# Kernel tuning notes

Hardware: AMD Instinct MI355X
Metric: run time of the kernel (lower is better)

## Reference

```python
import jax, jax.numpy as jnp
import numpy as np

B, N, DIM = 2, 2048, 512
H, DH = 8, 64
INNER = H * DH
SCALE = DH ** -0.5


def setup_inputs() -> dict:
    key = jax.random.key(0)
    ks = jax.random.split(key, 8)
    s = 0.02
    return {
        "nodes": jax.random.normal(ks[0], (B, N, DIM), dtype=jnp.float32),
        "edge_mask": jax.random.bernoulli(ks[1], 0.9, (B, N, N)),
        "wq": jax.random.normal(ks[2], (DIM, INNER), dtype=jnp.float32) * s,
        "bq": jnp.zeros((INNER,), dtype=jnp.float32),
        "wkv": jax.random.normal(ks[3], (DIM, 2 * INNER), dtype=jnp.float32) * s,
        "bkv": jnp.zeros((2 * INNER,), dtype=jnp.float32),
        "wo": jax.random.normal(ks[4], (INNER, DIM), dtype=jnp.float32) * s,
        "bo": jnp.zeros((DIM,), dtype=jnp.float32),
    }


def reference(nodes, edge_mask, wq, bq, wkv, bkv, wo, bo):
    b, n, _ = nodes.shape
    q = nodes @ wq + bq                      # [b, n, h*dh]
    kv = nodes @ wkv + bkv                   # [b, n, 2*h*dh]
    k, v = jnp.split(kv, 2, axis=-1)
    # split heads -> [b, h, n, dh]
    split = lambda t: t.reshape(b, n, H, DH).transpose(0, 2, 1, 3)
    q, k, v = split(q), split(k), split(v)
    sim = jnp.einsum('bhid,bhjd->bhij', q, k) * SCALE
    max_neg = -jnp.finfo(sim.dtype).max
    sim = jnp.where(edge_mask[:, None, :, :], sim, max_neg)
    attn = jax.nn.softmax(sim, axis=-1)
    out = jnp.einsum('bhij,bhjd->bhid', attn, v)      # [b, h, n, dh]
    out = out.transpose(0, 2, 1, 3).reshape(b, n, INNER)
    return out @ wo + bo
```

## Files before the change

### kernel.cpp

```cpp
#include <hip/hip_runtime.h>
#include <cstdint>
#include <cstddef>

#define DEVI __device__ __forceinline__

typedef __bf16 bf16x8 __attribute__((ext_vector_type(8)));
typedef float floatx4 __attribute__((ext_vector_type(4)));
typedef unsigned short us4v __attribute__((ext_vector_type(4)));
typedef unsigned short us8 __attribute__((ext_vector_type(8)));

static_assert(sizeof(bf16x8) == 16, "bf16x8 must be 16B");
static_assert(sizeof(us8) == 16, "us8 must be 16B");


#if __has_builtin(__builtin_amdgcn_cvt_pk_bf16_f32)
DEVI unsigned short f2bf(float f) {
  typedef __bf16 bf16x2 __attribute__((ext_vector_type(2)));
  union { bf16x2 v; unsigned short u[2]; } c;
  c.v = __builtin_amdgcn_cvt_pk_bf16_f32(f, 0.f);
  return c.u[0];
}
#else
DEVI unsigned short f2bf(float f) {
  unsigned int u = __float_as_uint(f);
  u += 0x7fffu + ((u >> 16) & 1u);
  return (unsigned short)(u >> 16);
}
#endif

DEVI float exp2c(float x) {
#if __has_builtin(__builtin_amdgcn_exp2f)
  return __builtin_amdgcn_exp2f(x);
#else
  return exp2f(x);
#endif
}

DEVI bf16x8 ld8(const unsigned short* p) { return *(const bf16x8*)p; }

typedef const __attribute__((address_space(1))) void* gas_ptr;
typedef __attribute__((address_space(3))) void* las_ptr;

DEVI void gld16(const void* g, void* l) {
  __builtin_amdgcn_global_load_lds((gas_ptr)g, (las_ptr)l, 16, 0, 0);
}

#define WAIT_LGKM0() __builtin_amdgcn_s_waitcnt(0xc07f)

__global__ __launch_bounds__(256) void prep_k(
    const float* __restrict__ nodes, const void* __restrict__ mask,
    const float* __restrict__ wq, const float* __restrict__ wkv,
    const float* __restrict__ wo,
    unsigned short* __restrict__ XB, unsigned short* __restrict__ WQKVT,
    unsigned short* __restrict__ WOT, unsigned int* __restrict__ pm) {
  int bid = blockIdx.x;
  if (bid < 8192) {
    __shared__ int mode;
    const unsigned int* md = (const unsigned int*)mask;
    unsigned int probe = md[threadIdx.x];
    bool odd = (probe > 1u && probe != 0x3f800000u);
    if (threadIdx.x == 0) mode = 0;
    __syncthreads();
    if (odd) atomicOr(&mode, 1);
    __syncthreads();
    int byteMode = mode;
    int t = bid * 256 + threadIdx.x;
    int lane = threadIdx.x & 63;
    unsigned int n;
    if (byteMode) {
      unsigned int x = md[t];
      n = ((x & 0xffu) ? 1u : 0u) | ((x & 0xff00u) ? 2u : 0u) |
          ((x & 0xff0000u) ? 4u : 0u) | ((x >> 24) ? 8u : 0u);
    } else {
      uint4 v = ((const uint4*)mask)[t];
      n = (v.x ? 1u : 0u) | (v.y ? 2u : 0u) | (v.z ? 4u : 0u) | (v.w ? 8u : 0u);
    }
    unsigned int w = n << ((lane & 7) * 4);
    w |= __shfl_xor(w, 1);
    w |= __shfl_xor(w, 2);
    w |= __shfl_xor(w, 4);
    if ((lane & 7) == 0) pm[t >> 3] = w;
  } else if (bid < 10240) {
    int i = (bid - 8192) * 256 + threadIdx.x;
    float4 v = ((const float4*)nodes)[i];
    us4v o;
    o[0] = f2bf(v.x); o[1] = f2bf(v.y); o[2] = f2bf(v.z); o[3] = f2bf(v.w);
    *(us4v*)(XB + (size_t)i * 4) = o;
  } else {
    int tb = bid - 10240;
    int x = tb & 15, y = (tb >> 4) & 7, z = tb >> 7;
    const float* src; unsigned short* dst; int C, c0;
    if (z == 0)      { if (x >= 8) return; src = wq;  dst = WQKVT; C = 512;  c0 = 0; }
    else if (z == 1) { src = wkv; dst = WQKVT; C = 1024; c0 = 512; }
    else             { if (x >= 8) return; src = wo;  dst = WOT;  C = 512;  c0 = 0; }
    __shared__ unsigned short t2[64 * 64];
    const int t = threadIdx.x;
    const int ct = x * 64, rt = y * 64;
    for (int p = 0; p < 4; p++) {
      int kl = p * 16 + (t >> 4);
      int cc = (t & 15) * 4;
      float4 v = *(const float4*)&src[(size_t)(rt + kl) * C + ct + cc];
      float f[4] = {v.x, v.y, v.z, v.w};
      for (int i = 0; i < 4; i++) {
        int c = cc + i;
        t2[c * 64 + (kl ^ (c & 56))] = f2bf(f[i]);
      }
    }
    __syncthreads();
    for (int p = 0; p < 2; p++) {
      int c = p * 32 + (t >> 3);
      int kc = (t & 7) * 8;
      us8 v = *(const us8*)&t2[c * 64 + (kc ^ (c & 56))];
      *(us8*)&dst[(size_t)(c0 + ct + c) * 512 + rt + kc] = v;
    }
  }
}

__global__ __launch_bounds__(256) void gemm_qkv_k(
    const unsigned short* __restrict__ A,
    const unsigned short* __restrict__ Bt,
    const float* __restrict__ bq, const float* __restrict__ bkv,
    unsigned short* __restrict__ Qo, unsigned short* __restrict__ Ko,
    unsigned short* __restrict__ VTo) {
  __shared__ unsigned short smem[8192];
  unsigned short* sA = smem;
  unsigned short* sB = smem + 2048;
  const int tid = threadIdx.x;
  const int wave = tid >> 6, lane = tid & 63, quad = lane >> 4, l16 = lane & 15;
  const int wm = wave >> 1, wn = wave & 1;
  const int bm = blockIdx.x, bn = blockIdx.y;
  floatx4 acc[2][4] = {};
  const int arow = lane >> 2;
  const int ag = lane & 3;
  for (int kt = 0; kt < 16; kt++) {
    __syncthreads();
    {
      int rowA = wave * 16 + arow;
      int gA = ag ^ (rowA & 3);
      gld16(&A[(size_t)(bm * 64 + rowA) * 512 + kt * 32 + gA * 8], &sA[(wave * 16) * 32]);
      for (int p = 0; p < 2; p++) {
        int rowB = p * 64 + wave * 16 + arow;
        int gB = ag ^ (rowB & 3);
        gld16(&Bt[(size_t)(bn * 128 + rowB) * 512 + kt * 32 + gB * 8],
              &sB[(p * 64 + wave * 16) * 32]);
      }
    }
    __syncthreads();
    bf16x8 aF[2], bF[4];
    int swz = (quad ^ (l16 & 3)) * 8;
    for (int i = 0; i < 2; i++) aF[i] = ld8(&sA[(wm * 32 + i * 16 + l16) * 32 + swz]);
    for (int j = 0; j < 4; j++) bF[j] = ld8(&sB[(wn * 64 + j * 16 + l16) * 32 + swz]);
    for (int i = 0; i < 2; i++)
      for (int j = 0; j < 4; j++)
        acc[i][j] = __builtin_amdgcn_mfma_f32_16x16x32_bf16(aF[i], bF[j], acc[i][j], 0, 0, 0);
  }

  const int sec = bn * 2 + wn;
  float bias[4];
  float scale = 1.0f;
  if (sec < 8) {
    for (int j = 0; j < 4; j++) bias[j] = bq[sec * 64 + j * 16 + l16];
    scale = 0.18033688011112042f;
  } else {
    for (int j = 0; j < 4; j++) bias[j] = bkv[(sec - 8) * 64 + j * 16 + l16];
  }
  const int gr0 = bm * 64 + wm * 32;
  const int b = gr0 >> 11, n0 = gr0 & 2047;
  unsigned short* pw = smem + wave * 2048;
  __syncthreads();
  if (sec < 16) {
    for (int i = 0; i < 2; i++)
      for (int j = 0; j < 4; j++) {
        int cg = j * 2 + (l16 >> 3), ci = l16 & 7;
        for (int r = 0; r < 4; r++) {
          int row = i * 16 + quad * 4 + r;
          pw[row * 64 + ((cg ^ (row & 7)) * 8) + ci] = f2bf((acc[i][j][r] + bias[j]) * scale);
        }
      }
    WAIT_LGKM0();
    unsigned short* dst = (sec < 8) ? Qo + ((size_t)(b * 8 + sec) * 2048 + n0) * 64
                                    : Ko + ((size_t)(b * 8 + sec - 8) * 2048 + n0) * 64;
    for (int p = 0; p < 4; p++) {
      int row = p * 8 + (lane >> 3);
      int c8 = lane & 7;
      us8 v = *(const us8*)&pw[row * 64 + ((c8 ^ (row & 7)) * 8)];
      *(us8*)&dst[(size_t)row * 64 + c8 * 8] = v;
    }
  } else {
    for (int i = 0; i < 2; i++)
      for (int j = 0; j < 4; j++) {
        int d = j * 16 + l16;
        us4v t;
        for (int r = 0; r < 4; r++) t[r] = f2bf(acc[i][j][r] + bias[j]);
        *(us4v*)&pw[d * 32 + ((quad ^ (d & 3)) * 8) + i * 4] = t;
      }
    WAIT_LGKM0();
    unsigned short* dst = VTo + (size_t)(b * 8 + sec - 16) * 64 * 2048 + n0;
    for (int p = 0; p < 4; p++) {
      int d = p * 16 + (lane >> 2);
      int c4 = lane & 3;
      us8 v = *(const us8*)&pw[d * 32 + ((c4 ^ (d & 3)) * 8)];
      *(us8*)&dst[(size_t)d * 2048 + c4 * 8] = v;
    }
  }
}

__global__ __launch_bounds__(256, 2) void attn_k(
    const unsigned short* __restrict__ Q,
    const unsigned short* __restrict__ K,
    const unsigned short* __restrict__ Vt,
    const unsigned int* __restrict__ pm,
    unsigned short* __restrict__ AO) {
  __shared__ unsigned short kT[4][4096];
  __shared__ unsigned short vT[4][4096];
  __shared__ float lsumB[4][64];
  const int tid = threadIdx.x;
  const int wave = tid >> 6, lane = tid & 63, quad = lane >> 4, l16 = lane & 15;
  const int bh = blockIdx.x, qt = blockIdx.y, b = bh >> 3, h = bh & 7;
  const int q0 = qt * 64;
  const unsigned short* Qb = Q + (size_t)bh * 2048 * 64;
  const unsigned short* Kb = K + (size_t)bh * 2048 * 64;
  const unsigned short* Vb = Vt + (size_t)bh * 64 * 2048;
  const unsigned int* pmB = pm + (size_t)b * 2048 * 64;

  bf16x8 qF[4][2];
  for (int qb = 0; qb < 4; qb++) {
    qF[qb][0] = ld8(&Qb[(size_t)(q0 + qb * 16 + l16) * 64 + quad * 8]);
    qF[qb][1] = ld8(&Qb[(size_t)(q0 + qb * 16 + l16) * 64 + 32 + quad * 8]);
  }

  floatx4 oacc[4][4] = {};
  float lsum[4] = {0.f, 0.f, 0.f, 0.f};

  const int srow = lane >> 3;
  const int gK = (lane & 7) ^ srow;
  const int rsw0 = quad ^ (l16 & 7);
  const int rsw1 = (4 + quad) ^ (l16 & 7);

  for (int it = 0; it < 8; ++it) {
    const int k0w = it * 256 + wave * 64;
    for (int p = 0; p < 8; p++) {
      gld16(&Kb[(size_t)(k0w + p * 8 + srow) * 64 + gK * 8], &kT[wave][p * 512]);
      gld16(&Vb[(size_t)(p * 8 + srow) * 2048 + k0w + gK * 8], &vT[wave][p * 512]);
    }
    uint2 mw[4];
    for (int qb = 0; qb < 4; qb++)
      mw[qb] = *(const uint2*)&pmB[(size_t)(q0 + qb * 16 + l16) * 64 + it * 8 + wave * 2];
    __syncthreads();

    for (int c = 0; c < 2; c++) {
      floatx4 st[4][2];
      for (int k2 = 0; k2 < 2; k2++) {
        const unsigned short* kr = &kT[wave][((c * 2 + k2) * 16 + l16) * 64];
        bf16x8 kf0 = ld8(kr + rsw0 * 8);
        bf16x8 kf1 = ld8(kr + rsw1 * 8);
        for (int qb = 0; qb < 4; qb++) {
          floatx4 z = {0.f, 0.f, 0.f, 0.f};
          z = __builtin_amdgcn_mfma_f32_16x16x32_bf16(kf0, qF[qb][0], z, 0, 0, 0);
          st[qb][k2] = __builtin_amdgcn_mfma_f32_16x16x32_bf16(kf1, qF[qb][1], z, 0, 0, 0);
        }
      }
      union uB { bf16x8 v; unsigned short u[8]; } pf[4];
      for (int qb = 0; qb < 4; qb++) {
        unsigned int w = c ? mw[qb].y : mw[qb].x;
        for (int k2 = 0; k2 < 2; k2++) {
          int base = k2 * 16 + quad * 4;
          for (int r = 0; r < 4; r++) {
            float e = exp2c(st[qb][k2][r]);
            e = ((w >> (base + r)) & 1u) ? e : 0.f;
            lsum[qb] += e;
            pf[qb].u[k2 * 4 + r] = f2bf(e);
          }
        }
      }
      for (int db = 0; db < 4; db++) {
        int row = db * 16 + l16;
        bf16x8 va = ld8(&vT[wave][row * 64 + (((c * 4 + quad) ^ (row & 7)) * 8)]);
        for (int qb = 0; qb < 4; qb++)
          oacc[db][qb] =
              __builtin_amdgcn_mfma_f32_16x16x32_bf16(va, pf[qb].v, oacc[db][qb], 0, 0, 0);
      }
    }
    __syncthreads();
  }

  for (int qb = 0; qb < 4; qb++) {
    lsum[qb] += __shfl_xor(lsum[qb], 16);
    lsum[qb] += __shfl_xor(lsum[qb], 32);
  }
  lsumB[wave][quad * 16 + l16] = lsum[quad];

  float* pO = (float*)&kT[0][0];
  float* myR = pO + wave * 4096;
  for (int db = 0; db < 4; db++)
    for (int qb = 0; qb < 4; qb++) {
      int q = qb * 16 + l16;
      *(floatx4*)&myR[q * 64 + (((db * 4 + quad) ^ l16) & 15) * 4] = oacc[db][qb];
    }
  __syncthreads();
  {
    int q = tid >> 2, dblk = tid & 3;
    float inv = 1.0f / (lsumB[0][q] + lsumB[1][q] + lsumB[2][q] + lsumB[3][q]);
    float o[16];
    for (int i = 0; i < 4; i++) {
      int dg = dblk * 4 + i;
      int off = q * 64 + ((dg ^ q) & 15) * 4;
      floatx4 s = *(floatx4*)&pO[off];
      s += *(floatx4*)&pO[4096 + off];
      s += *(floatx4*)&pO[8192 + off];
      s += *(floatx4*)&pO[12288 + off];
      for (int r = 0; r < 4; r++) o[i * 4 + r] = s[r] * inv;
    }
    us8 v0, v1;
    for (int i = 0; i < 8; i++) { v0[i] = f2bf(o[i]); v1[i] = f2bf(o[8 + i]); }
    unsigned short* dst = &AO[((size_t)b * 2048 + q0 + q) * 512 + h * 64 + dblk * 16];
    *(us8*)dst = v0;
    *(us8*)(dst + 8) = v1;
  }
}

__global__ __launch_bounds__(256) void gemm_out_k(
    const unsigned short* __restrict__ A,
    const unsigned short* __restrict__ Bt,
    const float* __restrict__ bo, float* __restrict__ out) {
  __shared__ unsigned short smem[6144];
  unsigned short* sA = smem;
  unsigned short* sB = smem + 2048;
  const int tid = threadIdx.x;
  const int wave = tid >> 6, lane = tid & 63, quad = lane >> 4, l16 = lane & 15;
  const int wm = wave >> 1, wn = wave & 1;
  const int bm = blockIdx.x, bn = blockIdx.y;
  floatx4 acc[2][4] = {};
  const int arow = lane >> 2;
  const int ag = lane & 3;
  for (int kt = 0; kt < 16; kt++) {
    __syncthreads();
    {
      int rowA = wave * 16 + arow;
      int gA = ag ^ (rowA & 3);
      gld16(&A[(size_t)(bm * 64 + rowA) * 512 + kt * 32 + gA * 8], &sA[(wave * 16) * 32]);
      for (int p = 0; p < 2; p++) {
        int rowB = p * 64 + wave * 16 + arow;
        int gB = ag ^ (rowB & 3);
        gld16(&Bt[(size_t)(bn * 128 + rowB) * 512 + kt * 32 + gB * 8],
              &sB[(p * 64 + wave * 16) * 32]);
      }
    }
    __syncthreads();
    bf16x8 aF[2], bF[4];
    int swz = (quad ^ (l16 & 3)) * 8;
    for (int i = 0; i < 2; i++) aF[i] = ld8(&sA[(wm * 32 + i * 16 + l16) * 32 + swz]);
    for (int j = 0; j < 4; j++) bF[j] = ld8(&sB[(wn * 64 + j * 16 + l16) * 32 + swz]);
    for (int i = 0; i < 2; i++)
      for (int j = 0; j < 4; j++)
        acc[i][j] = __builtin_amdgcn_mfma_f32_16x16x32_bf16(aF[i], bF[j], acc[i][j], 0, 0, 0);
  }
  for (int i = 0; i < 2; i++)
    for (int j = 0; j < 4; j++) {
      int gc = bn * 128 + wn * 64 + j * 16 + l16;
      float bb = bo[gc];
      for (int r = 0; r < 4; r++) {
        int gr = bm * 64 + wm * 32 + i * 16 + quad * 4 + r;
        out[(size_t)gr * 512 + gc] = acc[i][j][r] + bb;
      }
    }
}

extern "C" void kernel_launch(void* const* d_in, const int* in_sizes, int n_in,
                              void* d_out, int out_size, void* d_ws, size_t ws_size,
                              hipStream_t stream) {
  const float* nodes = (const float*)d_in[0];
  const void*  mask  = d_in[1];
  const float* wq    = (const float*)d_in[2];
  const float* bq    = (const float*)d_in[3];
  const float* wkv   = (const float*)d_in[4];
  const float* bkv   = (const float*)d_in[5];
  const float* wo    = (const float*)d_in[6];
  const float* bo    = (const float*)d_in[7];
  float* out = (float*)d_out;

  char* ws = (char*)d_ws;
  unsigned short* XB    = (unsigned short*)(ws + 0);
  unsigned short* WQKVT = (unsigned short*)(ws + 4194304);
  unsigned short* WOT   = (unsigned short*)(ws + 5767168);
  unsigned short* Qm    = (unsigned short*)(ws + 6291456);
  unsigned short* Km    = (unsigned short*)(ws + 10485760);
  unsigned short* VTm   = (unsigned short*)(ws + 18874368);
  unsigned short* AOm   = (unsigned short*)(ws + 23068672);
  unsigned int*   PM    = (unsigned int*)(ws + 27262976);

  prep_k<<<10624, 256, 0, stream>>>(nodes, mask, wq, wkv, wo, XB, WQKVT, WOT, PM);
  gemm_qkv_k<<<dim3(64, 12), 256, 0, stream>>>(XB, WQKVT, bq, bkv, Qm, Km, VTm);
  attn_k<<<dim3(16, 32), 256, 0, stream>>>(Qm, Km, VTm, PM, AOm);
  gemm_out_k<<<dim3(64, 4), 256, 0, stream>>>(AOm, WOT, bo, out);
}
```

Baseline: 153.5 us.

## Double-buffer LDS staging in GEMM and attention kernels, pack bf16 conversions

The QKV and output GEMMs now prefetch the next K-tile into a second LDS buffer while the current tile is multiplied, which removes one barrier per iteration. The attention kernel moves to 16 iterations of 32 keys per wave, double-buffered, so K/V loads overlap the QK^T, softmax and PV work, with a new V swizzle for the narrower tile. Softmax probabilities are converted two at a time with the packed bf16 instruction. The cost is more LDS per block in the GEMMs and more, smaller attention iterations, each with its own mask load and barrier.

```diff
diff --git a/kernel.cpp b/kernel.cpp
--- a/kernel.cpp
+++ b/kernel.cpp
@@ -5,26 +5,33 @@
 #define DEVI __device__ __forceinline__
 
 typedef __bf16 bf16x8 __attribute__((ext_vector_type(8)));
+typedef __bf16 bf16x2 __attribute__((ext_vector_type(2)));
 typedef float floatx4 __attribute__((ext_vector_type(4)));
 typedef unsigned short us4v __attribute__((ext_vector_type(4)));
 typedef unsigned short us8 __attribute__((ext_vector_type(8)));
 
 static_assert(sizeof(bf16x8) == 16, "bf16x8 must be 16B");
-static_assert(sizeof(us8) == 16, "us8 must be 16B");
 
 
 #if __has_builtin(__builtin_amdgcn_cvt_pk_bf16_f32)
 DEVI unsigned short f2bf(float f) {
-  typedef __bf16 bf16x2 __attribute__((ext_vector_type(2)));
   union { bf16x2 v; unsigned short u[2]; } c;
   c.v = __builtin_amdgcn_cvt_pk_bf16_f32(f, 0.f);
   return c.u[0];
+}
+DEVI unsigned int pk2bf(float a, float b) {
+  union { bf16x2 v; unsigned int u; } c;
+  c.v = __builtin_amdgcn_cvt_pk_bf16_f32(a, b);
+  return c.u;
 }
 #else
 DEVI unsigned short f2bf(float f) {
   unsigned int u = __float_as_uint(f);
   u += 0x7fffu + ((u >> 16) & 1u);
   return (unsigned short)(u >> 16);
+}
+DEVI unsigned int pk2bf(float a, float b) {
+  return (unsigned int)f2bf(a) | ((unsigned int)f2bf(b) << 16);
 }
 #endif
 
@@ -122,9 +129,7 @@
     const float* __restrict__ bq, const float* __restrict__ bkv,
     unsigned short* __restrict__ Qo, unsigned short* __restrict__ Ko,
     unsigned short* __restrict__ VTo) {
-  __shared__ unsigned short smem[8192];
-  unsigned short* sA = smem;
-  unsigned short* sB = smem + 2048;
+  __shared__ unsigned short smem[12288];
   const int tid = threadIdx.x;
   const int wave = tid >> 6, lane = tid & 63, quad = lane >> 4, l16 = lane & 15;
   const int wm = wave >> 1, wn = wave & 1;
@@ -132,20 +137,27 @@
   floatx4 acc[2][4] = {};
   const int arow = lane >> 2;
   const int ag = lane & 3;
+
+  auto stage = [&](int kt, int buf) {
+    unsigned short* sA = smem + buf * 6144;
+    unsigned short* sB = sA + 2048;
+    int rowA = wave * 16 + arow;
+    int gA = ag ^ (rowA & 3);
+    gld16(&A[(size_t)(bm * 64 + rowA) * 512 + kt * 32 + gA * 8], &sA[(wave * 16) * 32]);
+    for (int p = 0; p < 2; p++) {
+      int rowB = p * 64 + wave * 16 + arow;
+      int gB = ag ^ (rowB & 3);
+      gld16(&Bt[(size_t)(bn * 128 + rowB) * 512 + kt * 32 + gB * 8],
+            &sB[(p * 64 + wave * 16) * 32]);
+    }
+  };
+
+  stage(0, 0);
   for (int kt = 0; kt < 16; kt++) {
     __syncthreads();
-    {
-      int rowA = wave * 16 + arow;
-      int gA = ag ^ (rowA & 3);
-      gld16(&A[(size_t)(bm * 64 + rowA) * 512 + kt * 32 + gA * 8], &sA[(wave * 16) * 32]);
-      for (int p = 0; p < 2; p++) {
-        int rowB = p * 64 + wave * 16 + arow;
-        int gB = ag ^ (rowB & 3);
-        gld16(&Bt[(size_t)(bn * 128 + rowB) * 512 + kt * 32 + gB * 8],
-              &sB[(p * 64 + wave * 16) * 32]);
-      }
-    }
-    __syncthreads();
+    if (kt + 1 < 16) stage(kt + 1, (kt + 1) & 1);
+    const unsigned short* sA = smem + (kt & 1) * 6144;
+    const unsigned short* sB = sA + 2048;
     bf16x8 aF[2], bF[4];
     int swz = (quad ^ (l16 & 3)) * 8;
     for (int i = 0; i < 2; i++) aF[i] = ld8(&sA[(wm * 32 + i * 16 + l16) * 32 + swz]);
@@ -211,8 +223,7 @@
     const unsigned short* __restrict__ Vt,
     const unsigned int* __restrict__ pm,
     unsigned short* __restrict__ AO) {
-  __shared__ unsigned short kT[4][4096];
-  __shared__ unsigned short vT[4][4096];
+  __shared__ unsigned short smem[32768];
   __shared__ float lsumB[4][64];
   const int tid = threadIdx.x;
   const int wave = tid >> 6, lane = tid & 63, quad = lane >> 4, l16 = lane & 15;
@@ -232,57 +243,77 @@
   floatx4 oacc[4][4] = {};
   float lsum[4] = {0.f, 0.f, 0.f, 0.f};
 
-  const int srow = lane >> 3;
-  const int gK = (lane & 7) ^ srow;
+  const int krow = lane >> 3;
+  const int kg = (lane & 7) ^ krow;
+  const int vrow = lane >> 2;
+  const int vpos = lane & 3;
+
+  auto stage = [&](int it, int buf) {
+    const int k0w = it * 128 + wave * 32;
+    unsigned short* kTw = smem + buf * 16384 + wave * 2048;
+    unsigned short* vTw = smem + buf * 16384 + 8192 + wave * 2048;
+    for (int p = 0; p < 4; p++) {
+      int row = p * 8 + krow;
+      gld16(&Kb[(size_t)(k0w + row) * 64 + kg * 8], &kTw[p * 512]);
+      int d = p * 16 + vrow;
+      int gsrc = vpos ^ ((d >> 1) & 3);
+      gld16(&Vb[(size_t)d * 2048 + k0w + gsrc * 8], &vTw[p * 512]);
+    }
+  };
+
+  stage(0, 0);
   const int rsw0 = quad ^ (l16 & 7);
   const int rsw1 = (4 + quad) ^ (l16 & 7);
 
-  for (int it = 0; it < 8; ++it) {
-    const int k0w = it * 256 + wave * 64;
-    for (int p = 0; p < 8; p++) {
-      gld16(&Kb[(size_t)(k0w + p * 8 + srow) * 64 + gK * 8], &kT[wave][p * 512]);
-      gld16(&Vb[(size_t)(p * 8 + srow) * 2048 + k0w + gK * 8], &vT[wave][p * 512]);
-    }
-    uint2 mw[4];
+  for (int it = 0; it < 16; ++it) {
+    const int buf = it & 1;
+    __syncthreads();
+    if (it + 1 < 16) stage(it + 1, buf ^ 1);
+
+    const unsigned short* kTw = smem + buf * 16384 + wave * 2048;
+    const unsigned short* vTw = smem + buf * 16384 + 8192 + wave * 2048;
+
+    unsigned int mw[4];
     for (int qb = 0; qb < 4; qb++)
-      mw[qb] = *(const uint2*)&pmB[(size_t)(q0 + qb * 16 + l16) * 64 + it * 8 + wave * 2];
-    __syncthreads();
-
-    for (int c = 0; c < 2; c++) {
-      floatx4 st[4][2];
+      mw[qb] = pmB[(size_t)(q0 + qb * 16 + l16) * 64 + it * 4 + wave];
+
+    floatx4 st[4][2];
+    for (int k2 = 0; k2 < 2; k2++) {
+      const unsigned short* kr = &kTw[(k2 * 16 + l16) * 64];
+      bf16x8 kf0 = ld8(kr + rsw0 * 8);
+      bf16x8 kf1 = ld8(kr + rsw1 * 8);
+      for (int qb = 0; qb < 4; qb++) {
+        floatx4 z = {0.f, 0.f, 0.f, 0.f};
+        z = __builtin_amdgcn_mfma_f32_16x16x32_bf16(kf0, qF[qb][0], z, 0, 0, 0);
+        st[qb][k2] = __builtin_amdgcn_mfma_f32_16x16x32_bf16(kf1, qF[qb][1], z, 0, 0, 0);
+      }
+    }
+
+    union uB { bf16x8 v; unsigned int d[4]; } pf[4];
+    for (int qb = 0; qb < 4; qb++) {
+      unsigned int w = mw[qb];
       for (int k2 = 0; k2 < 2; k2++) {
-        const unsigned short* kr = &kT[wave][((c * 2 + k2) * 16 + l16) * 64];
-        bf16x8 kf0 = ld8(kr + rsw0 * 8);
-        bf16x8 kf1 = ld8(kr + rsw1 * 8);
-        for (int qb = 0; qb < 4; qb++) {
-          floatx4 z = {0.f, 0.f, 0.f, 0.f};
-          z = __builtin_amdgcn_mfma_f32_16x16x32_bf16(kf0, qF[qb][0], z, 0, 0, 0);
-          st[qb][k2] = __builtin_amdgcn_mfma_f32_16x16x32_bf16(kf1, qF[qb][1], z, 0, 0, 0);
-        }
-      }
-      union uB { bf16x8 v; unsigned short u[8]; } pf[4];
-      for (int qb = 0; qb < 4; qb++) {
-        unsigned int w = c ? mw[qb].y : mw[qb].x;
-        for (int k2 = 0; k2 < 2; k2++) {
-          int base = k2 * 16 + quad * 4;
-          for (int r = 0; r < 4; r++) {
-            float e = exp2c(st[qb][k2][r]);
-            e = ((w >> (base + r)) & 1u) ? e : 0.f;
-            lsum[qb] += e;
-            pf[qb].u[k2 * 4 + r] = f2bf(e);
-          }
-        }
-      }
-      for (int db = 0; db < 4; db++) {
-        int row = db * 16 + l16;
-        bf16x8 va = ld8(&vT[wave][row * 64 + (((c * 4 + quad) ^ (row & 7)) * 8)]);
-        for (int qb = 0; qb < 4; qb++)
-          oacc[db][qb] =
-              __builtin_amdgcn_mfma_f32_16x16x32_bf16(va, pf[qb].v, oacc[db][qb], 0, 0, 0);
-      }
-    }
-    __syncthreads();
-  }
+        int base = k2 * 16 + quad * 4;
+        float e0 = exp2c(st[qb][k2][0]); e0 = ((w >> (base + 0)) & 1u) ? e0 : 0.f;
+        float e1 = exp2c(st[qb][k2][1]); e1 = ((w >> (base + 1)) & 1u) ? e1 : 0.f;
+        float e2 = exp2c(st[qb][k2][2]); e2 = ((w >> (base + 2)) & 1u) ? e2 : 0.f;
+        float e3 = exp2c(st[qb][k2][3]); e3 = ((w >> (base + 3)) & 1u) ? e3 : 0.f;
+        lsum[qb] += (e0 + e1) + (e2 + e3);
+        pf[qb].d[k2 * 2]     = pk2bf(e0, e1);
+        pf[qb].d[k2 * 2 + 1] = pk2bf(e2, e3);
+      }
+    }
+
+    for (int db = 0; db < 4; db++) {
+      int row = db * 16 + l16;
+      int pos = quad ^ ((row >> 1) & 3);
+      bf16x8 va = ld8(&vTw[row * 32 + pos * 8]);
+      for (int qb = 0; qb < 4; qb++)
+        oacc[db][qb] =
+            __builtin_amdgcn_mfma_f32_16x16x32_bf16(va, pf[qb].v, oacc[db][qb], 0, 0, 0);
+    }
+  }
+  __syncthreads();
 
   for (int qb = 0; qb < 4; qb++) {
     lsum[qb] += __shfl_xor(lsum[qb], 16);
@@ -290,7 +321,7 @@
   }
   lsumB[wave][quad * 16 + l16] = lsum[quad];
 
-  float* pO = (float*)&kT[0][0];
+  float* pO = (float*)smem;
   float* myR = pO + wave * 4096;
   for (int db = 0; db < 4; db++)
     for (int qb = 0; qb < 4; qb++) {
@@ -323,9 +354,7 @@
     const unsigned short* __restrict__ A,
     const unsigned short* __restrict__ Bt,
     const float* __restrict__ bo, float* __restrict__ out) {
-  __shared__ unsigned short smem[6144];
-  unsigned short* sA = smem;
-  unsigned short* sB = smem + 2048;
+  __shared__ unsigned short smem[12288];
   const int tid = threadIdx.x;
   const int wave = tid >> 6, lane = tid & 63, quad = lane >> 4, l16 = lane & 15;
   const int wm = wave >> 1, wn = wave & 1;
@@ -333,20 +362,27 @@
   floatx4 acc[2][4] = {};
   const int arow = lane >> 2;
   const int ag = lane & 3;
+
+  auto stage = [&](int kt, int buf) {
+    unsigned short* sA = smem + buf * 6144;
+    unsigned short* sB = sA + 2048;
+    int rowA = wave * 16 + arow;
+    int gA = ag ^ (rowA & 3);
+    gld16(&A[(size_t)(bm * 64 + rowA) * 512 + kt * 32 + gA * 8], &sA[(wave * 16) * 32]);
+    for (int p = 0; p < 2; p++) {
+      int rowB = p * 64 + wave * 16 + arow;
+      int gB = ag ^ (rowB & 3);
+      gld16(&Bt[(size_t)(bn * 128 + rowB) * 512 + kt * 32 + gB * 8],
+            &sB[(p * 64 + wave * 16) * 32]);
+    }
+  };
+
+  stage(0, 0);
   for (int kt = 0; kt < 16; kt++) {
     __syncthreads();
-    {
-      int rowA = wave * 16 + arow;
-      int gA = ag ^ (rowA & 3);
-      gld16(&A[(size_t)(bm * 64 + rowA) * 512 + kt * 32 + gA * 8], &sA[(wave * 16) * 32]);
-      for (int p = 0; p < 2; p++) {
-        int rowB = p * 64 + wave * 16 + arow;
-        int gB = ag ^ (rowB & 3);
-        gld16(&Bt[(size_t)(bn * 128 + rowB) * 512 + kt * 32 + gB * 8],
-              &sB[(p * 64 + wave * 16) * 32]);
-      }
-    }
-    __syncthreads();
+    if (kt + 1 < 16) stage(kt + 1, (kt + 1) & 1);
+    const unsigned short* sA = smem + (kt & 1) * 6144;
+    const unsigned short* sB = sA + 2048;
     bf16x8 aF[2], bF[4];
     int swz = (quad ^ (l16 & 3)) * 8;
     for (int i = 0; i < 2; i++) aF[i] = ld8(&sA[(wm * 32 + i * 16 + l16) * 32 + swz]);
```

Result: no change. 156.1 us (+1.7%).
